# Kernel optimization log

Measured on AMD Instinct MI355X. Metric: run time of the kernel, lower is better.

Reference implementation:

```python
import jax, jax.numpy as jnp
import numpy as np

B, T, X, H, Z = 64, 2048, 128, 256, 64


def setup_inputs() -> dict:
    key = jax.random.key(0)
    ks = jax.random.split(key, 6)
    s = lambda n: 1.0 / np.sqrt(n).astype(np.float32)
    return {
        "x_seq": jax.random.normal(ks[0], (B, T, X), jnp.float32),
        # LSTMCell params packed as [i|f|g|o] gates. Flax: input dense has no bias,
        # hidden dense has bias.
        "Wi": jax.random.normal(ks[1], (X, 4 * H), jnp.float32) * s(X),
        "Wh": jax.random.normal(ks[2], (H, 4 * H), jnp.float32) * s(H),
        "bh": jnp.zeros((4 * H,), jnp.float32),
        # head: Dense(H) -> relu -> Dense(2Z)
        "W1": jax.random.normal(ks[3], (H, H), jnp.float32) * s(H),
        "b1": jnp.zeros((H,), jnp.float32),
        "W2": jax.random.normal(ks[4], (H, 2 * Z), jnp.float32) * s(H),
        "b2": jnp.zeros((2 * Z,), jnp.float32),
    }


def _forward(x_seq, Wi, Wh, bh, W1, b1, W2, b2):
    Bsz = x_seq.shape[0]
    Hd = Wh.shape[0]
    # Precompute input projection for all timesteps (one big GEMM).
    x_proj = jnp.einsum('btx,xg->btg', x_seq, Wi)  # (B, T, 4H)
    xp = jnp.swapaxes(x_proj, 0, 1)  # (T, B, 4H) for scan

    def step(carry, xp_t):
        c, h = carry
        gates = xp_t + h @ Wh + bh  # (B, 4H)
        i, f, g, o = jnp.split(gates, 4, axis=-1)
        i = jax.nn.sigmoid(i)
        f = jax.nn.sigmoid(f)
        g = jnp.tanh(g)
        o = jax.nn.sigmoid(o)
        c = f * c + i * g
        h = o * jnp.tanh(c)
        hid = jax.nn.relu(h @ W1 + b1)
        out = hid @ W2 + b2  # (B, 2Z)
        return (c, h), out

    c0 = jnp.zeros((Bsz, Hd), x_seq.dtype)
    h0 = jnp.zeros((Bsz, Hd), x_seq.dtype)
    _, outs = jax.lax.scan(step, (c0, h0), xp)  # outs: (T, B, 2Z)
    outs = jnp.swapaxes(outs, 0, 1)  # (B, T, 2Z)
    mu_seq, log_sigma_seq = jnp.split(outs, 2, axis=-1)
    return mu_seq, log_sigma_seq


def reference(x_seq, Wi, Wh, bh, W1, b1, W2, b2):
    return _forward(x_seq, Wi, Wh, bh, W1, b1, W2, b2)
```

## Files before the change

kernel.cpp:

```cpp
#include <hip/hip_runtime.h>

typedef _Float16 f16;
typedef _Float16 h2 __attribute__((ext_vector_type(2)));
typedef _Float16 h8 __attribute__((ext_vector_type(8)));
typedef float f4 __attribute__((ext_vector_type(4)));

constexpr int Bb = 64, Tt = 2048, Xx = 128, Hh = 256, G4 = 1024, Z2 = 128;

__device__ __forceinline__ float fdot2f(h2 a, h2 b, float c) {
#if __has_builtin(__builtin_amdgcn_fdot2)
  return __builtin_amdgcn_fdot2(a, b, c, false);
#else
  return c + (float)a[0] * (float)b[0] + (float)a[1] * (float)b[1];
#endif
}
__device__ __forceinline__ float tanhf_(float x) {
  float e = __expf(2.0f * x);
  return 1.0f - 2.0f * __builtin_amdgcn_rcpf(e + 1.0f);
}
__device__ __forceinline__ h2 bch2(unsigned int u) { return __builtin_bit_cast(h2, u); }

template <int CTRL>
__device__ __forceinline__ float qb(float v) {
  return __builtin_bit_cast(float,
      __builtin_amdgcn_mov_dpp(__builtin_bit_cast(int, v), CTRL, 0xf, 0xf, true));
}
__device__ __forceinline__ float qsum(float v) {
  v += qb<0xB1>(v);
  v += qb<0x4E>(v);
  return v;
}

__global__ void cast_f16_k(const float* __restrict__ in, f16* __restrict__ out, int n) {
  int i = (blockIdx.x * 256 + threadIdx.x) * 4;
  if (i >= n) return;
  float4 v = *(const float4*)(in + i);
  h2 a = {(f16)v.x, (f16)v.y};
  h2 b = {(f16)v.z, (f16)v.w};
  uint2 o = {__builtin_bit_cast(unsigned int, a), __builtin_bit_cast(unsigned int, b)};
  *(uint2*)(out + i) = o;
}

__global__ void cast_whT_k(const float* __restrict__ Wh, f16* __restrict__ WhT) {
  int idx = blockIdx.x * 256 + threadIdx.x;
  int tid = idx >> 8, r = idx & 255;
  int s = r >> 1, e = r & 1;
  int half = s >> 6, gate = (s >> 4) & 3, kk = s & 15;
  int j = tid >> 2, q = tid & 3;
  int k = q * 64 + half * 32 + kk * 2 + e;
  WhT[idx] = (f16)Wh[(long)k * G4 + gate * 256 + j];
}

__global__ __launch_bounds__(256, 4) void gemm_f16_k(
    const f16* __restrict__ A, const f16* __restrict__ Bm, const float* __restrict__ bias,
    f16* __restrict__ C16, float* __restrict__ Cmu, float* __restrict__ Cls,
    int N, int K, int a_shift, int a_ostride, int a_t0,
    int mode, int o_t0, int tcshift)
{
  __shared__ __align__(16) f16 At[64][48];
  __shared__ __align__(16) f16 Bt[64][48];
  const int tid = threadIdx.x;
  const int mblk = blockIdx.x, nblk = blockIdx.y;
  const int w = tid >> 6, lane = tid & 63;

  const int sa_row = tid >> 2, sa_k = (tid & 3) * 8;
  const int m_g = mblk * 64 + sa_row;
  const long arow = (long)(m_g >> a_shift) * a_ostride + a_t0 + (m_g & ((1 << a_shift) - 1));
  const f16* aptr = A + arow * K + sa_k;
  const int sb_k = tid >> 3, sb_n = (tid & 7) * 8;
  const f16* bptr = Bm + (long)sb_k * N + nblk * 64 + sb_n;

  f4 acc[4];
#pragma unroll
  for (int i = 0; i < 4; ++i) acc[i] = (f4){0.f, 0.f, 0.f, 0.f};

  const int arow_l = w * 16 + (lane & 15);
  const int k0 = (lane >> 4) * 8;

  for (int kk = 0; kk < K; kk += 32) {
    uint4 av = *(const uint4*)(aptr + kk);
    uint4 bv = *(const uint4*)(bptr + (long)kk * N);
    __syncthreads();
    *(uint4*)&At[sa_row][sa_k] = av;
    h8 bx = __builtin_bit_cast(h8, bv);
#pragma unroll
    for (int j = 0; j < 8; ++j) Bt[sb_n + j][sb_k] = bx[j];
    __syncthreads();
    h8 af = *(const h8*)&At[arow_l][k0];
#pragma unroll
    for (int nt = 0; nt < 4; ++nt) {
      h8 bf = *(const h8*)&Bt[nt * 16 + (lane & 15)][k0];
      acc[nt] = __builtin_amdgcn_mfma_f32_16x16x32_f16(af, bf, acc[nt], 0, 0, 0);
    }
  }

  const int row_l = w * 16 + ((lane >> 4) << 2);
  const int col_l = lane & 15;
#pragma unroll
  for (int nt = 0; nt < 4; ++nt) {
    int gcol = nblk * 64 + nt * 16 + col_l;
    float bv = bias[gcol];
#pragma unroll
    for (int r = 0; r < 4; ++r) {
      int gm = mblk * 64 + row_l + r;
      float val = acc[nt][r] + bv;
      if (mode == 1) val = fmaxf(val, 0.f);
      if (mode <= 1) {
        C16[(long)gm * N + gcol] = (f16)val;
      } else {
        int bb = gm >> tcshift, tl = gm & ((1 << tcshift) - 1);
        long orow = (long)bb * Tt + o_t0 + tl;
        if (gcol < 64) Cmu[orow * 64 + gcol] = val;
        else Cls[orow * 64 + (gcol - 64)] = val;
      }
    }
  }
}

__global__ void __launch_bounds__(1024, 4) lstm_rec_k(
    const f16* __restrict__ WhT, const f16* __restrict__ xp,
    f16* __restrict__ hout, float* __restrict__ c_state, f16* __restrict__ h_state,
    int TC, int first)
{
  const int b = blockIdx.x, tid = threadIdx.x;
  const int j = tid >> 2, q = tid & 3;
  __shared__ __align__(16) h2 hbuf[2][4][36];
  __shared__ __align__(16) h2 wlds[9][1024][4];

  h2 w[92];
  {
    const uint4* p4 = (const uint4*)(WhT + (long)tid * 256);
#pragma unroll
    for (int i = 0; i < 23; ++i) {
      uint4 v = p4[i];
      w[4 * i + 0] = bch2(v.x); w[4 * i + 1] = bch2(v.y);
      w[4 * i + 2] = bch2(v.z); w[4 * i + 3] = bch2(v.w);
    }
#pragma unroll
    for (int gg = 0; gg < 9; ++gg) *(uint4*)&wlds[gg][tid][0] = p4[23 + gg];
  }

  float c = first ? 0.f : c_state[b * Hh + j];
  if (tid < 128) {
    h2 hz = {(f16)0.f, (f16)0.f};
    hbuf[0][tid >> 5][tid & 31] = first ? hz : ((const h2*)h_state)[b * 128 + tid];
  }
  __syncthreads();

  const float sgn = (q == 2) ? 2.0f : -1.0f;
  const int xcol = (q << 8) | j;
  const f16* xptr = xp + (long)b * TC * G4 + xcol;
  const f16* xend = xptr + (long)(TC - 1) * G4;
  f16 xc = *xptr;
  int p = 0;
  for (int t = 0; t < TC; ++t) {
    const f16* xnp = (xptr == xend) ? xptr : xptr + G4;
    f16 xn = *xnp;

    const uint4* hq = (const uint4*)&hbuf[p][q][0];
    float d0 = 0.f, d1 = 0.f, d2 = 0.f, d3 = 0.f;
    {
      uint4 ha = hq[0], hb_ = hq[1], hc = hq[2], hd = hq[3];
      h2 hh0[16] = {bch2(ha.x),  bch2(ha.y),  bch2(ha.z),  bch2(ha.w),
                    bch2(hb_.x), bch2(hb_.y), bch2(hb_.z), bch2(hb_.w),
                    bch2(hc.x),  bch2(hc.y),  bch2(hc.z),  bch2(hc.w),
                    bch2(hd.x),  bch2(hd.y),  bch2(hd.z),  bch2(hd.w)};
#pragma unroll
      for (int m = 0; m < 16; ++m) {
        d0 = fdot2f(w[m], hh0[m], d0);
        d1 = fdot2f(w[16 + m], hh0[m], d1);
        d2 = fdot2f(w[32 + m], hh0[m], d2);
        d3 = fdot2f(w[48 + m], hh0[m], d3);
      }
    }
    {
      uint4 ha = hq[4], hb_ = hq[5], hc = hq[6], hd = hq[7];
      h2 hh1[16] = {bch2(ha.x),  bch2(ha.y),  bch2(ha.z),  bch2(ha.w),
                    bch2(hb_.x), bch2(hb_.y), bch2(hb_.z), bch2(hb_.w),
                    bch2(hc.x),  bch2(hc.y),  bch2(hc.z),  bch2(hc.w),
                    bch2(hd.x),  bch2(hd.y),  bch2(hd.z),  bch2(hd.w)};
#pragma unroll
      for (int m = 0; m < 16; ++m) d0 = fdot2f(w[64 + m], hh1[m], d0);
#pragma unroll
      for (int m = 0; m < 12; ++m) d1 = fdot2f(w[80 + m], hh1[m], d1);
      {
        uint4 wv = *(const uint4*)&wlds[0][tid][0];
        d1 = fdot2f(bch2(wv.x), hh1[12], d1);
        d1 = fdot2f(bch2(wv.y), hh1[13], d1);
        d1 = fdot2f(bch2(wv.z), hh1[14], d1);
        d1 = fdot2f(bch2(wv.w), hh1[15], d1);
      }
#pragma unroll
      for (int gg = 1; gg <= 4; ++gg) {
        uint4 wv = *(const uint4*)&wlds[gg][tid][0];
        int m0 = 4 * (gg - 1);
        d2 = fdot2f(bch2(wv.x), hh1[m0 + 0], d2);
        d2 = fdot2f(bch2(wv.y), hh1[m0 + 1], d2);
        d2 = fdot2f(bch2(wv.z), hh1[m0 + 2], d2);
        d2 = fdot2f(bch2(wv.w), hh1[m0 + 3], d2);
      }
#pragma unroll
      for (int gg = 5; gg <= 8; ++gg) {
        uint4 wv = *(const uint4*)&wlds[gg][tid][0];
        int m0 = 4 * (gg - 5);
        d3 = fdot2f(bch2(wv.x), hh1[m0 + 0], d3);
        d3 = fdot2f(bch2(wv.y), hh1[m0 + 1], d3);
        d3 = fdot2f(bch2(wv.z), hh1[m0 + 2], d3);
        d3 = fdot2f(bch2(wv.w), hh1[m0 + 3], d3);
      }
    }

    d0 = qsum(d0); d1 = qsum(d1); d2 = qsum(d2); d3 = qsum(d3);
    float a = (q & 1) ? d1 : d0;
    float b2_ = (q & 1) ? d3 : d2;
    a = (q & 2) ? b2_ : a;
    a += (float)xc;

    float e = __expf(sgn * a);
    float r = __builtin_amdgcn_rcpf(1.0f + e);
    float act = (q == 2) ? 1.0f - 2.0f * r : r;

    float ai = qb<0x00>(act), af = qb<0x55>(act);
    float ag = qb<0xAA>(act), ao = qb<0xFF>(act);
    c = af * c + ai * ag;
    float hval = ao * tanhf_(c);
    if (q == 3) {
      f16 hh = (f16)hval;
      ((f16*)&hbuf[p ^ 1][0][0])[(j >> 6) * 72 + (j & 63)] = hh;
      hout[((long)b * TC + t) * Hh + j] = hh;
    }
    __syncthreads();
    p ^= 1;
    xc = xn;
    xptr = xnp;
  }
  if (q == 0) c_state[b * Hh + j] = c;
  if (tid < 128) ((h2*)h_state)[b * 128 + tid] = hbuf[p][tid >> 5][tid & 31];
}

extern "C" void kernel_launch(void* const* d_in, const int* in_sizes, int n_in,
                              void* d_out, int out_size, void* d_ws, size_t ws_size,
                              hipStream_t stream)
{
  const float* x  = (const float*)d_in[0];
  const float* Wi = (const float*)d_in[1];
  const float* Wh = (const float*)d_in[2];
  const float* bh = (const float*)d_in[3];
  const float* W1 = (const float*)d_in[4];
  const float* b1 = (const float*)d_in[5];
  const float* W2 = (const float*)d_in[6];
  const float* b2 = (const float*)d_in[7];
  float* out = (float*)d_out;

  char* ws = (char*)d_ws;
  size_t off = 0;
  auto alloc = [&](size_t bytes) -> char* {
    char* p = ws + off;
    off = (off + bytes + 255) & ~(size_t)255;
    return p;
  };
  f16* x16   = (f16*)alloc((size_t)Bb * Tt * Xx * 2);
  f16* wi16  = (f16*)alloc((size_t)Xx * G4 * 2);
  f16* whT16 = (f16*)alloc((size_t)G4 * Hh * 2);
  f16* w116  = (f16*)alloc((size_t)Hh * Hh * 2);
  f16* w216  = (f16*)alloc((size_t)Hh * Z2 * 2);
  float* cst = (float*)alloc((size_t)Bb * Hh * 4);
  f16* hst   = (f16*)alloc((size_t)Bb * Hh * 2);

  int tc = 2048;
  while (tc > 32) {
    size_t need = (size_t)Bb * tc * G4 * 2 + (size_t)Bb * tc * Hh * 2;
    if (off + need <= ws_size) break;
    tc >>= 1;
  }
  int tcsh = __builtin_ctz((unsigned)tc);
  f16* xp16 = (f16*)alloc((size_t)Bb * tc * G4 * 2);
  f16* h16  = (f16*)alloc((size_t)Bb * tc * Hh * 2);
  f16* hid16 = xp16;

  cast_f16_k<<<(Bb * Tt * Xx) / 1024, 256, 0, stream>>>(x, x16, Bb * Tt * Xx);
  cast_f16_k<<<(Xx * G4) / 1024, 256, 0, stream>>>(Wi, wi16, Xx * G4);
  cast_f16_k<<<(Hh * Hh) / 1024, 256, 0, stream>>>(W1, w116, Hh * Hh);
  cast_f16_k<<<(Hh * Z2) / 1024, 256, 0, stream>>>(W2, w216, Hh * Z2);
  cast_whT_k<<<(Hh * G4) / 256, 256, 0, stream>>>(Wh, whT16);

  float* mu = out;
  float* ls = out + (size_t)Bb * Tt * 64;

  for (int t0 = 0; t0 < Tt; t0 += tc) {
    dim3 gx(Bb * tc / 64, G4 / 64);
    gemm_f16_k<<<gx, 256, 0, stream>>>(x16, wi16, bh, xp16, nullptr, nullptr,
                                       G4, Xx, tcsh, Tt, t0, 0, 0, 0);
    lstm_rec_k<<<Bb, 1024, 0, stream>>>(whT16, xp16, h16, cst, hst, tc, (t0 == 0) ? 1 : 0);
    dim3 g1g(Bb * tc / 64, Hh / 64);
    gemm_f16_k<<<g1g, 256, 0, stream>>>(h16, w116, b1, hid16, nullptr, nullptr,
                                        Hh, Hh, 30, 0, 0, 1, 0, 0);
    dim3 g2g(Bb * tc / 64, Z2 / 64);
    gemm_f16_k<<<g2g, 256, 0, stream>>>(hid16, w216, b2, nullptr, mu, ls,
                                        Z2, Hh, 30, 0, 0, 2, t0, tcsh);
  }
}
```

Before: 3.566 ms.

## Add 512-thread LSTM recurrence kernel with two gate columns per thread

Adds a recurrence kernel where each of 512 threads computes two gate pre-activations per hidden unit, keeping most Wh weights in registers and the rest in LDS, with a new weight-packing cast. The time chunk drops to 1024 so the first chunk runs the new kernel and the second runs the old 1024-thread kernel. This aims to cut per-step cross-thread shuffling and barrier cost, at the price of higher register pressure, an extra chunk of launches, and an extra weight conversion pass.

```diff
diff --git a/kernel.cpp b/kernel.cpp
--- a/kernel.cpp
+++ b/kernel.cpp
@@ -49,6 +49,20 @@
   int j = tid >> 2, q = tid & 3;
   int k = q * 64 + half * 32 + kk * 2 + e;
   WhT[idx] = (f16)Wh[(long)k * G4 + gate * 256 + j];
+}
+
+__global__ void cast_whT2_k(const float* __restrict__ Wh, f16* __restrict__ WhT2) {
+  int idx = blockIdx.x * 256 + threadIdx.x;
+  int tid = idx >> 9, f = idx & 511;
+  int s = f >> 1, e = f & 1;
+  int c_off, k;
+  if (s < 96)      { c_off = 0; k = 2 * s + e; }
+  else if (s < 192){ c_off = 1; k = 2 * (s - 96) + e; }
+  else if (s < 224){ c_off = 0; k = 192 + 2 * (s - 192) + e; }
+  else             { c_off = 1; k = 192 + 2 * (s - 224) + e; }
+  int cc = 2 * tid + c_off;
+  int j = cc >> 2, g = cc & 3;
+  WhT2[(long)tid * 512 + f] = (f16)Wh[(long)k * G4 + g * 256 + j];
 }
 
 __global__ __launch_bounds__(256, 4) void gemm_f16_k(
@@ -115,6 +129,108 @@
       }
     }
   }
+}
+
+__global__ void __launch_bounds__(512, 2) lstm512_k(
+    const f16* __restrict__ WhT2, const f16* __restrict__ xp,
+    f16* __restrict__ hout, float* __restrict__ c_state, f16* __restrict__ h_state,
+    int TC, int first)
+{
+  const int b = blockIdx.x, tid = threadIdx.x;
+  const int j = tid >> 1, odd = tid & 1;
+  __shared__ __align__(16) h2 hbuf[2][128];
+  __shared__ uint4 wt[16][512];
+
+  h2 w[192];
+  {
+    const uint4* p4 = (const uint4*)(WhT2 + (long)tid * 512);
+#pragma unroll
+    for (int u = 0; u < 48; ++u) {
+      uint4 v = p4[u];
+      w[4 * u + 0] = bch2(v.x); w[4 * u + 1] = bch2(v.y);
+      w[4 * u + 2] = bch2(v.z); w[4 * u + 3] = bch2(v.w);
+    }
+#pragma unroll
+    for (int gg = 0; gg < 16; ++gg) wt[gg][tid] = p4[48 + gg];
+  }
+
+  float c = first ? 0.f : c_state[b * Hh + j];
+  if (tid < 128) {
+    h2 hz = {(f16)0.f, (f16)0.f};
+    hbuf[0][tid] = first ? hz : ((const h2*)h_state)[b * 128 + tid];
+  }
+  __syncthreads();
+
+  const float sgn0 = odd ? 2.0f : -1.0f;
+  const int xcol0 = (odd * 2) * 256 + j;
+  const int xcol1 = xcol0 + 256;
+  const f16* xbase = xp + (long)b * TC * G4;
+  const f16* xptr0 = xbase + xcol0;
+  const f16* xptr1 = xbase + xcol1;
+  const f16* xend0 = xptr0 + (long)(TC - 1) * G4;
+  f16 xc0 = *xptr0, xc1 = *xptr1;
+  int p = 0;
+  for (int t = 0; t < TC; ++t) {
+    bool last = (xptr0 == xend0);
+    const f16* xn0p = last ? xptr0 : xptr0 + G4;
+    const f16* xn1p = last ? xptr1 : xptr1 + G4;
+    f16 xn0 = *xn0p, xn1 = *xn1p;
+
+    float a0 = (float)xc0, b0 = 0.f, a1 = (float)xc1, b1 = 0.f;
+    const uint4* hb4 = (const uint4*)&hbuf[p][0];
+#pragma unroll
+    for (int i = 0; i < 24; ++i) {
+      uint4 hv = hb4[i];
+      a0 = fdot2f(w[4 * i + 0], bch2(hv.x), a0);
+      b0 = fdot2f(w[4 * i + 1], bch2(hv.y), b0);
+      a0 = fdot2f(w[4 * i + 2], bch2(hv.z), a0);
+      b0 = fdot2f(w[4 * i + 3], bch2(hv.w), b0);
+      a1 = fdot2f(w[96 + 4 * i + 0], bch2(hv.x), a1);
+      b1 = fdot2f(w[96 + 4 * i + 1], bch2(hv.y), b1);
+      a1 = fdot2f(w[96 + 4 * i + 2], bch2(hv.z), a1);
+      b1 = fdot2f(w[96 + 4 * i + 3], bch2(hv.w), b1);
+    }
+#pragma unroll
+    for (int gg = 0; gg < 8; ++gg) {
+      uint4 hv = hb4[24 + gg];
+      uint4 wa = wt[gg][tid];
+      uint4 wb = wt[8 + gg][tid];
+      a0 = fdot2f(bch2(wa.x), bch2(hv.x), a0);
+      b0 = fdot2f(bch2(wa.y), bch2(hv.y), b0);
+      a0 = fdot2f(bch2(wa.z), bch2(hv.z), a0);
+      b0 = fdot2f(bch2(wa.w), bch2(hv.w), b0);
+      a1 = fdot2f(bch2(wb.x), bch2(hv.x), a1);
+      b1 = fdot2f(bch2(wb.y), bch2(hv.y), b1);
+      a1 = fdot2f(bch2(wb.z), bch2(hv.z), a1);
+      b1 = fdot2f(bch2(wb.w), bch2(hv.w), b1);
+    }
+    float A0 = a0 + b0, A1 = a1 + b1;
+
+    float e0 = __expf(sgn0 * A0);
+    float r0 = __builtin_amdgcn_rcpf(1.0f + e0);
+    float act0 = odd ? 1.0f - 2.0f * r0 : r0;
+    float e1 = __expf(-A1);
+    float act1 = __builtin_amdgcn_rcpf(1.0f + e1);
+
+    float px0 = qb<0xB1>(act0), px1 = qb<0xB1>(act1);
+    float ai = odd ? px0 : act0;
+    float af = odd ? px1 : act1;
+    float ag = odd ? act0 : px0;
+    float ao = odd ? act1 : px1;
+    c = af * c + ai * ag;
+    float hval = ao * tanhf_(c);
+    if (!odd) {
+      f16 hh = (f16)hval;
+      ((f16*)&hbuf[p ^ 1][0])[j] = hh;
+      hout[((long)b * TC + t) * Hh + j] = hh;
+    }
+    __syncthreads();
+    p ^= 1;
+    xc0 = xn0; xc1 = xn1;
+    xptr0 = xn0p; xptr1 = xn1p;
+  }
+  if (!odd) c_state[b * Hh + j] = c;
+  if (tid < 128) ((h2*)h_state)[b * 128 + tid] = hbuf[p][tid];
 }
 
 __global__ void __launch_bounds__(1024, 4) lstm_rec_k(
@@ -262,12 +378,13 @@
   f16* x16   = (f16*)alloc((size_t)Bb * Tt * Xx * 2);
   f16* wi16  = (f16*)alloc((size_t)Xx * G4 * 2);
   f16* whT16 = (f16*)alloc((size_t)G4 * Hh * 2);
+  f16* whT2  = (f16*)alloc((size_t)G4 * Hh * 2);
   f16* w116  = (f16*)alloc((size_t)Hh * Hh * 2);
   f16* w216  = (f16*)alloc((size_t)Hh * Z2 * 2);
   float* cst = (float*)alloc((size_t)Bb * Hh * 4);
   f16* hst   = (f16*)alloc((size_t)Bb * Hh * 2);
 
-  int tc = 2048;
+  int tc = 1024;
   while (tc > 32) {
     size_t need = (size_t)Bb * tc * G4 * 2 + (size_t)Bb * tc * Hh * 2;
     if (off + need <= ws_size) break;
@@ -283,15 +400,20 @@
   cast_f16_k<<<(Hh * Hh) / 1024, 256, 0, stream>>>(W1, w116, Hh * Hh);
   cast_f16_k<<<(Hh * Z2) / 1024, 256, 0, stream>>>(W2, w216, Hh * Z2);
   cast_whT_k<<<(Hh * G4) / 256, 256, 0, stream>>>(Wh, whT16);
+  cast_whT2_k<<<(Hh * G4) / 256, 256, 0, stream>>>(Wh, whT2);
 
   float* mu = out;
   float* ls = out + (size_t)Bb * Tt * 64;
 
-  for (int t0 = 0; t0 < Tt; t0 += tc) {
+  int ci = 0;
+  for (int t0 = 0; t0 < Tt; t0 += tc, ++ci) {
     dim3 gx(Bb * tc / 64, G4 / 64);
     gemm_f16_k<<<gx, 256, 0, stream>>>(x16, wi16, bh, xp16, nullptr, nullptr,
                                        G4, Xx, tcsh, Tt, t0, 0, 0, 0);
-    lstm_rec_k<<<Bb, 1024, 0, stream>>>(whT16, xp16, h16, cst, hst, tc, (t0 == 0) ? 1 : 0);
+    if (ci == 0)
+      lstm512_k<<<Bb, 512, 0, stream>>>(whT2, xp16, h16, cst, hst, tc, (t0 == 0) ? 1 : 0);
+    else
+      lstm_rec_k<<<Bb, 1024, 0, stream>>>(whT16, xp16, h16, cst, hst, tc, (t0 == 0) ? 1 : 0);
     dim3 g1g(Bb * tc / 64, Hh / 64);
     gemm_f16_k<<<g1g, 256, 0, stream>>>(h16, w116, b1, hid16, nullptr, nullptr,
                                         Hh, Hh, 30, 0, 0, 1, 0, 0);
```

Result: faster. 3.354 ms (-6.0%).
